# Kernel tuning notes

Measured on AMD Instinct MI355X. Metric: run time of the kernel, lower is better.

Reference implementation:

```python
import jax, jax.numpy as jnp
import numpy as np

N = 100000
E = 3200000
IN_C = 512
HID = 64
OP_C = 64
OUT_C = 2


def setup_inputs() -> dict:
    key = jax.random.key(0)
    ks = jax.random.split(key, 12)
    x = jax.random.normal(ks[0], (N, IN_C), dtype=jnp.float32)
    edge_index = jax.random.randint(ks[1], (2, E), 0, N, dtype=jnp.int32)
    edge_attr = jax.random.uniform(ks[2], (E,), dtype=jnp.float32)
    op = jax.random.normal(ks[3], (N, OP_C), dtype=jnp.float32)
    s1 = 1.0 / np.sqrt(IN_C)
    s2 = 1.0 / np.sqrt(HID)
    s3 = 1.0 / np.sqrt(IN_C + OP_C)
    W1 = jax.random.uniform(ks[4], (IN_C, HID), jnp.float32, -s1, s1)
    b1 = jnp.zeros((HID,), jnp.float32)
    W2 = jax.random.uniform(ks[5], (HID, HID), jnp.float32, -s2, s2)
    b2 = jnp.zeros((HID,), jnp.float32)
    Wp = jax.random.uniform(ks[6], (HID, IN_C), jnp.float32, -s2, s2)
    bp = jax.random.uniform(ks[7], (IN_C,), jnp.float32, -s2, s2)
    Wfc = jax.random.uniform(ks[8], (IN_C + OP_C, OUT_C), jnp.float32, -s3, s3)
    bfc = jax.random.uniform(ks[9], (OUT_C,), jnp.float32, -s3, s3)
    return {"x": x, "edge_index": edge_index, "edge_attr": edge_attr, "op": op,
            "W1": W1, "b1": b1, "W2": W2, "b2": b2,
            "Wp": Wp, "bp": bp, "Wfc": Wfc, "bfc": bfc}


def _gcn_conv(x, W, b, row, col, w):
    # PyG GCNConv: add self-loops (weight 1), symmetric normalization,
    # messages flow source(row) -> target(col).
    h = x @ W  # [N, out]
    loop = jnp.arange(N, dtype=row.dtype)
    row_f = jnp.concatenate([row, loop])
    col_f = jnp.concatenate([col, loop])
    w_f = jnp.concatenate([w, jnp.ones((N,), w.dtype)])
    deg = jax.ops.segment_sum(w_f, col_f, num_segments=N)
    dinv = jnp.where(deg > 0, jax.lax.rsqrt(jnp.maximum(deg, 1e-30)), 0.0)
    norm = dinv[row_f] * w_f * dinv[col_f]  # [E+N]
    msg = norm[:, None] * h[row_f]          # gather + weight
    out = jax.ops.segment_sum(msg, col_f, num_segments=N)  # scatter-add
    return out + b


def reference(x, edge_index, edge_attr, op, W1, b1, W2, b2, Wp, bp, Wfc, bfc):
    row, col = edge_index[0], edge_index[1]
    w = 1.0 / (edge_attr + 1.0)
    h = jax.nn.relu(_gcn_conv(x, W1, b1, row, col, w))   # dropout = identity (eval)
    h = jax.nn.relu(_gcn_conv(h, W2, b2, row, col, w))
    emb = h @ Wp + bp
    z = jnp.concatenate([emb, op], axis=1)
    return z @ Wfc + bfc
```

## Files before the change

kernel.cpp:

```cpp
#include <hip/hip_runtime.h>
#include <hip/hip_bf16.h>

#define IN_C 512
#define HID 64
#define OP_C 64
#define OUT_C 2

#define NPB 256
#define NPB_SHIFT 8
#define MAXB 512
#define BINB 1024
#define EPT 8
#define EPB (BINB*EPT)
#define WFIX 16777216.0f

using bf16x8 = __attribute__((ext_vector_type(8))) short;
using f32x4  = __attribute__((ext_vector_type(4))) float;

static __device__ __forceinline__ unsigned short f2bf(float f) {
    unsigned int u = __float_as_uint(f);
    u = (u + 0x7FFFu + ((u >> 16) & 1u)) >> 16;
    return (unsigned short)u;
}
static __device__ __forceinline__ short f2bf_hw(float f) {
    __bf16 h = (__bf16)f;
    return __builtin_bit_cast(short, h);
}
static __device__ __forceinline__ float bf2f(unsigned short s) {
    return __uint_as_float(((unsigned int)s) << 16);
}

static __device__ __forceinline__ unsigned long long pack_e(int src, int lc, float w) {
    return ((unsigned long long)lc << 49) | ((unsigned long long)(unsigned)src << 32)
         | (unsigned long long)__float_as_uint(w);
}

static __device__ __forceinline__ void wprep_one(const float* __restrict__ W,
                                                 unsigned short* __restrict__ wfrag, int idx) {
    int e  = idx & 7;
    int l  = (idx >> 3) & 63;
    int nf = (idx >> 9) & 3;
    int kt = idx >> 11;
    int k  = kt * 32 + (l >> 4) * 8 + e;
    int c  = nf * 16 + (l & 15);
    wfrag[idx] = f2bf(W[k * 64 + c]);
}

__global__ __launch_bounds__(256) void setup_k(const float* __restrict__ Wp,
                                               const float* __restrict__ bp,
                                               const float* __restrict__ Wfc,
                                               const float* __restrict__ bfc,
                                               float* M, float* cvec,
                                               const float* __restrict__ W1,
                                               unsigned short* __restrict__ wfrag1,
                                               const float* __restrict__ W2,
                                               unsigned short* __restrict__ wfrag2,
                                               int* gcnt, int B) {
    int b = blockIdx.x, t = threadIdx.x;
    if (b == 0) {
        if (t < 128) {
            int k = t >> 1, j = t & 1;
            float s = 0.f;
            for (int f = 0; f < IN_C; ++f) s += Wp[k * IN_C + f] * Wfc[f * 2 + j];
            M[t] = s;
        } else if (t < 130) {
            int j = t - 128;
            float s = bfc[j];
            for (int f = 0; f < IN_C; ++f) s += bp[f] * Wfc[f * 2 + j];
            cvec[j] = s;
        }
    } else if (b <= 128) {
        wprep_one(W1, wfrag1, (b - 1) * 256 + t);
    } else if (b <= 144) {
        wprep_one(W2, wfrag2, (b - 129) * 256 + t);
    } else {
        int i = (b - 145) * 256 + t;
        if (i < B) gcnt[i] = 0;
    }
}

__global__ __launch_bounds__(BINB) void p1a_k(const int* __restrict__ col,
                                              int* __restrict__ gcnt,
                                              int* __restrict__ blk_off,
                                              int E, int B) {
    __shared__ int hist[MAXB];
    int tid = threadIdx.x;
    long e0 = (long)blockIdx.x * EPB;
    for (int i = tid; i < B; i += BINB) hist[i] = 0;
    __syncthreads();
    #pragma unroll
    for (int j = 0; j < EPT; ++j) {
        long e = e0 + j * BINB + tid;
        if (e < E) atomicAdd(&hist[col[e] >> NPB_SHIFT], 1);
    }
    __syncthreads();
    for (int b = tid; b < B; b += BINB) {
        int h = hist[b];
        if (h > 0) blk_off[(long)blockIdx.x * B + b] = atomicAdd(&gcnt[b], h);
    }
}

__global__ __launch_bounds__(256) void scanB_k(const int* __restrict__ gcnt,
                                               int* __restrict__ bptr, int B, int E) {
    __shared__ int lds[256];
    int t = threadIdx.x;
    int v[4]; int s = 0;
    #pragma unroll
    for (int j = 0; j < 4; ++j) { int i = t * 4 + j; v[j] = (i < B) ? gcnt[i] : 0; s += v[j]; }
    lds[t] = s; __syncthreads();
    int x = s;
    for (int off = 1; off < 256; off <<= 1) {
        int y = (t >= off) ? lds[t - off] : 0;
        __syncthreads();
        x += y; lds[t] = x;
        __syncthreads();
    }
    int p = x - s;
    #pragma unroll
    for (int j = 0; j < 4; ++j) { int i = t * 4 + j; if (i < B) bptr[i] = p; p += v[j]; }
    if (t == 255) bptr[B] = E;
}

__global__ __launch_bounds__(BINB) void p1b_k(const int* __restrict__ row,
                                              const int* __restrict__ col,
                                              const float* __restrict__ attr,
                                              const int* __restrict__ blk_off,
                                              const int* __restrict__ bptr,
                                              unsigned long long* __restrict__ binned,
                                              int E, int B) {
    __shared__ int gbase[MAXB];
    __shared__ int loc[MAXB];
    __shared__ int scanb[512];
    __shared__ unsigned long long stage[EPB];
    int tid = threadIdx.x;
    int blk = blockIdx.x;
    long e0 = (long)blk * EPB;
    for (int i = tid; i < B; i += BINB) {
        gbase[i] = bptr[i] + blk_off[(long)blk * B + i];
        loc[i] = 0;
    }
    __syncthreads();
    unsigned long long pk[EPT]; int eb[EPT]; int er[EPT];
    #pragma unroll
    for (int j = 0; j < EPT; ++j) {
        long e = e0 + j * BINB + tid;
        eb[j] = -1;
        if (e < E) {
            int c = col[e];
            int b = c >> NPB_SHIFT;
            float w = 1.0f / (attr[e] + 1.0f);
            pk[j] = pack_e(row[e], c & (NPB - 1), w);
            eb[j] = b;
            er[j] = atomicAdd(&loc[b], 1);
        }
    }
    __syncthreads();
    if (tid < 512) scanb[tid] = (tid < B) ? loc[tid] : 0;
    __syncthreads();
    for (int off = 1; off < 512; off <<= 1) {
        int y = 0;
        if (tid < 512 && tid >= off) y = scanb[tid - off];
        __syncthreads();
        if (tid < 512) scanb[tid] += y;
        __syncthreads();
    }
    if (tid < B) loc[tid] = scanb[tid] - loc[tid];
    __syncthreads();
    #pragma unroll
    for (int j = 0; j < EPT; ++j)
        if (eb[j] >= 0) stage[loc[eb[j]] + er[j]] = pk[j];
    __syncthreads();
    long rem = E - e0;
    int ecnt = rem > EPB ? EPB : (int)rem;
    for (int i = tid; i < ecnt; i += BINB) {
        int lo = 0, hi = B - 1;
        #pragma unroll 1
        while (lo < hi) {
            int mid = (lo + hi + 1) >> 1;
            if (loc[mid] <= i) lo = mid; else hi = mid - 1;
        }
        binned[gbase[lo] + (i - loc[lo])] = stage[i];
    }
}

__global__ __launch_bounds__(256) void p2_k(const unsigned long long* __restrict__ binned,
                                            const int* __restrict__ bptr,
                                            int2* __restrict__ edges,
                                            int* __restrict__ rowptr,
                                            float* __restrict__ dinv,
                                            int N, int E) {
    __shared__ int cnt[NPB];
    __shared__ unsigned int fxw[NPB];
    __shared__ int excl[NPB];
    __shared__ int cur[NPB];
    __shared__ float dvl[NPB];
    int tid = threadIdx.x;
    int b = blockIdx.x;
    int e0 = bptr[b], e1 = bptr[b + 1];
    int c0 = b << NPB_SHIFT;
    cnt[tid] = 0; fxw[tid] = 0; cur[tid] = 0;
    if (b == 0 && tid == 0) rowptr[N] = E;
    __syncthreads();
    for (int i = e0 + tid; i < e1; i += 256) {
        unsigned long long p = binned[i];
        int lc = (int)(p >> 49);
        float w = __uint_as_float((unsigned int)p);
        atomicAdd(&cnt[lc], 1);
        atomicAdd(&fxw[lc], (unsigned int)(w * WFIX));
    }
    __syncthreads();
    excl[tid] = cnt[tid];
    __syncthreads();
    for (int off = 1; off < NPB; off <<= 1) {
        int v = (tid >= off) ? excl[tid - off] : 0;
        __syncthreads();
        excl[tid] += v;
        __syncthreads();
    }
    {
        int ex = excl[tid] - cnt[tid];
        excl[tid] = ex;
        int c = c0 + tid;
        if (c < N) {
            rowptr[c] = e0 + ex;
            float deg = 1.0f + (float)((double)fxw[tid] * (1.0 / 16777216.0));
            float dv = rsqrtf(deg);
            dinv[c] = dv;
            dvl[tid] = dv;
        }
    }
    __syncthreads();
    for (int i = e0 + tid; i < e1; i += 256) {
        unsigned long long p = binned[i];
        int lc = (int)(p >> 49);
        int src = (int)((p >> 32) & 0x1FFFF);
        float w = __uint_as_float((unsigned int)p);
        int r = atomicAdd(&cur[lc], 1);
        float nrm_p = w * dvl[lc];
        edges[e0 + excl[lc] + r] = make_int2(src, __float_as_int(nrm_p));
    }
}

__global__ __launch_bounds__(512) void gemm1_k(const float* __restrict__ A,
                                               const unsigned short* __restrict__ wfrag,
                                               const float* __restrict__ dinv,
                                               unsigned short* __restrict__ out, int M) {
    __shared__ unsigned short wlds[32768];
    int tid = threadIdx.x;
    {
        const float4* s4 = (const float4*)wfrag;
        float4* d4 = (float4*)wlds;
        #pragma unroll
        for (int i = 0; i < 8; ++i) d4[tid + 512 * i] = s4[tid + 512 * i];
    }
    __syncthreads();
    int wv = tid >> 6, l = tid & 63;
    int lg = l >> 4, lr = l & 15;
    long band = (long)blockIdx.x * 128 + wv * 16;
    long row = band + lr;
    long rowc = row < M ? row : (long)(M - 1);
    const float* xp = A + rowc * IN_C + lg * 8;
    f32x4 acc0 = {0.f,0.f,0.f,0.f}, acc1 = {0.f,0.f,0.f,0.f};
    f32x4 acc2 = {0.f,0.f,0.f,0.f}, acc3 = {0.f,0.f,0.f,0.f};
    #pragma unroll 4
    for (int kt = 0; kt < 16; ++kt) {
        float4 xa = *(const float4*)(xp + kt * 32);
        float4 xb = *(const float4*)(xp + kt * 32 + 4);
        bf16x8 a;
        a[0] = f2bf_hw(xa.x); a[1] = f2bf_hw(xa.y);
        a[2] = f2bf_hw(xa.z); a[3] = f2bf_hw(xa.w);
        a[4] = f2bf_hw(xb.x); a[5] = f2bf_hw(xb.y);
        a[6] = f2bf_hw(xb.z); a[7] = f2bf_hw(xb.w);
        const bf16x8* bp = (const bf16x8*)&wlds[kt * 4 * 64 * 8 + l * 8];
        acc0 = __builtin_amdgcn_mfma_f32_16x16x32_bf16(a, bp[0],   acc0, 0, 0, 0);
        acc1 = __builtin_amdgcn_mfma_f32_16x16x32_bf16(a, bp[64],  acc1, 0, 0, 0);
        acc2 = __builtin_amdgcn_mfma_f32_16x16x32_bf16(a, bp[128], acc2, 0, 0, 0);
        acc3 = __builtin_amdgcn_mfma_f32_16x16x32_bf16(a, bp[192], acc3, 0, 0, 0);
    }
    #pragma unroll
    for (int r = 0; r < 4; ++r) {
        long orow = band + lg * 4 + r;
        if (orow < M) {
            float dv = dinv[orow];
            out[orow * 64 +  0 + lr] = f2bf(acc0[r] * dv);
            out[orow * 64 + 16 + lr] = f2bf(acc1[r] * dv);
            out[orow * 64 + 32 + lr] = f2bf(acc2[r] * dv);
            out[orow * 64 + 48 + lr] = f2bf(acc3[r] * dv);
        }
    }
}

__global__ __launch_bounds__(512) void gemm2_k(const unsigned short* __restrict__ A2,
                                               const unsigned short* __restrict__ wfrag,
                                               const float* __restrict__ dinv,
                                               unsigned short* __restrict__ out, int M) {
    __shared__ unsigned short wlds[4096];
    int tid = threadIdx.x;
    ((float4*)wlds)[tid] = ((const float4*)wfrag)[tid];
    __syncthreads();
    int wv = tid >> 6, l = tid & 63;
    int lg = l >> 4, lr = l & 15;
    long band = (long)blockIdx.x * 128 + wv * 16;
    long row = band + lr;
    long rowc = row < M ? row : (long)(M - 1);
    const unsigned short* ap = A2 + rowc * 64 + lg * 8;
    f32x4 acc0 = {0.f,0.f,0.f,0.f}, acc1 = {0.f,0.f,0.f,0.f};
    f32x4 acc2 = {0.f,0.f,0.f,0.f}, acc3 = {0.f,0.f,0.f,0.f};
    #pragma unroll
    for (int kt = 0; kt < 2; ++kt) {
        bf16x8 a = *(const bf16x8*)(ap + kt * 32);
        const bf16x8* bp = (const bf16x8*)&wlds[kt * 4 * 64 * 8 + l * 8];
        acc0 = __builtin_amdgcn_mfma_f32_16x16x32_bf16(a, bp[0],   acc0, 0, 0, 0);
        acc1 = __builtin_amdgcn_mfma_f32_16x16x32_bf16(a, bp[64],  acc1, 0, 0, 0);
        acc2 = __builtin_amdgcn_mfma_f32_16x16x32_bf16(a, bp[128], acc2, 0, 0, 0);
        acc3 = __builtin_amdgcn_mfma_f32_16x16x32_bf16(a, bp[192], acc3, 0, 0, 0);
    }
    #pragma unroll
    for (int r = 0; r < 4; ++r) {
        long orow = band + lg * 4 + r;
        if (orow < M) {
            float dv = dinv[orow];
            out[orow * 64 +  0 + lr] = f2bf(acc0[r] * dv);
            out[orow * 64 + 16 + lr] = f2bf(acc1[r] * dv);
            out[orow * 64 + 32 + lr] = f2bf(acc2[r] * dv);
            out[orow * 64 + 48 + lr] = f2bf(acc3[r] * dv);
        }
    }
}

__device__ __forceinline__ void agg_core(const unsigned short* __restrict__ h2,
                                         const int* __restrict__ rowptr,
                                         const int2* __restrict__ edges,
                                         const float* __restrict__ dinv,
                                         const float* __restrict__ bias,
                                         int node, int l,
                                         float& acc0, float& acc1) {
    float di = dinv[node];
    ushort2 hv = *(const ushort2*)(h2 + (size_t)node * 64 + 2 * l);
    acc0 = di * bf2f(hv.x);
    acc1 = di * bf2f(hv.y);
    int s = rowptr[node], e = rowptr[node + 1];
    int li = l & 15;
    for (int base = s; base < e; base += 16) {
        int mm = e - base; mm = mm > 16 ? 16 : mm;
        int2 my = edges[base + (li < mm ? li : 0)];
        if (mm == 16) {
            #pragma unroll
            for (int j = 0; j < 16; ++j) {
                int srcj = __shfl(my.x, j, 32);
                float nj = __int_as_float(__shfl(my.y, j, 32));
                ushort2 q = *(const ushort2*)(h2 + (size_t)srcj * 64 + 2 * l);
                acc0 += nj * bf2f(q.x);
                acc1 += nj * bf2f(q.y);
            }
        } else {
            for (int j = 0; j < mm; ++j) {
                int srcj = __shfl(my.x, j, 32);
                float nj = __int_as_float(__shfl(my.y, j, 32));
                ushort2 q = *(const ushort2*)(h2 + (size_t)srcj * 64 + 2 * l);
                acc0 += nj * bf2f(q.x);
                acc1 += nj * bf2f(q.y);
            }
        }
    }
    float2 bb = *(const float2*)(bias + 2 * l);
    acc0 = fmaxf(acc0 + bb.x, 0.0f);
    acc1 = fmaxf(acc1 + bb.y, 0.0f);
}

__global__ __launch_bounds__(256) void agg1_k(const unsigned short* __restrict__ h2,
                                              unsigned short* __restrict__ g2,
                                              const int* __restrict__ rowptr,
                                              const int2* __restrict__ edges,
                                              const float* __restrict__ dinv,
                                              const float* __restrict__ bias, int N) {
    int wid = (blockIdx.x * 256 + threadIdx.x) >> 6;
    int lane = threadIdx.x & 63;
    int node = wid * 2 + (lane >> 5);
    int l = lane & 31;
    if (node >= N) return;
    float acc0, acc1;
    agg_core(h2, rowptr, edges, dinv, bias, node, l, acc0, acc1);
    ushort2 o; o.x = f2bf(acc0); o.y = f2bf(acc1);
    *(ushort2*)(g2 + (size_t)node * 64 + 2 * l) = o;
}

__global__ __launch_bounds__(256) void agg2f_k(const unsigned short* __restrict__ h2,
                                               const int* __restrict__ rowptr,
                                               const int2* __restrict__ edges,
                                               const float* __restrict__ dinv,
                                               const float* __restrict__ bias,
                                               const float* __restrict__ op,
                                               const float* __restrict__ M,
                                               const float* __restrict__ Wfc,
                                               const float* __restrict__ cvec,
                                               float* __restrict__ out, int N) {
    int wid = (blockIdx.x * 256 + threadIdx.x) >> 6;
    int lane = threadIdx.x & 63;
    int node = wid * 2 + (lane >> 5);
    int l = lane & 31;
    if (node >= N) return;
    float acc0, acc1;
    agg_core(h2, rowptr, edges, dinv, bias, node, l, acc0, acc1);
    float2 ov = *(const float2*)(op + (size_t)node * 64 + 2 * l);
    int f0 = 2 * l, f1 = 2 * l + 1;
    float p0 = acc0 * M[f0 * 2 + 0] + acc1 * M[f1 * 2 + 0]
             + ov.x * Wfc[(IN_C + f0) * 2 + 0] + ov.y * Wfc[(IN_C + f1) * 2 + 0];
    float p1 = acc0 * M[f0 * 2 + 1] + acc1 * M[f1 * 2 + 1]
             + ov.x * Wfc[(IN_C + f0) * 2 + 1] + ov.y * Wfc[(IN_C + f1) * 2 + 1];
    #pragma unroll
    for (int off = 16; off > 0; off >>= 1) {
        p0 += __shfl_xor(p0, off);
        p1 += __shfl_xor(p1, off);
    }
    if (l == 0)
        *(float2*)(out + (size_t)node * 2) = make_float2(p0 + cvec[0], p1 + cvec[1]);
}

extern "C" void kernel_launch(void* const* d_in, const int* in_sizes, int n_in,
                              void* d_out, int out_size, void* d_ws, size_t ws_size,
                              hipStream_t stream) {
    const float* x    = (const float*)d_in[0];
    const int*   ei   = (const int*)d_in[1];
    const float* attr = (const float*)d_in[2];
    const float* op   = (const float*)d_in[3];
    const float* W1   = (const float*)d_in[4];
    const float* b1   = (const float*)d_in[5];
    const float* W2   = (const float*)d_in[6];
    const float* b2   = (const float*)d_in[7];
    const float* Wp   = (const float*)d_in[8];
    const float* bp   = (const float*)d_in[9];
    const float* Wfc  = (const float*)d_in[10];
    const float* bfc  = (const float*)d_in[11];

    const int N = in_sizes[0] / IN_C;
    const int E = in_sizes[2];
    const int* row = ei;
    const int* col = ei + E;

    const int B     = (N + NPB - 1) >> NPB_SHIFT;
    const int nblk1 = (E + EPB - 1) / EPB;

    char* base = (char*)d_ws;
    size_t off = 0;
    auto alloc = [&](size_t bytes) -> char* {
        char* p = base + off;
        off = (off + bytes + 255) & ~(size_t)255;
        return p;
    };
    int2*  edges  = (int2*)alloc((size_t)E * 8);
    unsigned short* h2 = (unsigned short*)alloc((size_t)N * HID * 2);
    size_t bin_b  = (size_t)E * 8;
    size_t g_b    = (size_t)N * HID * 2;
    char*  regC   = alloc(bin_b > g_b ? bin_b : g_b);
    unsigned long long* binned = (unsigned long long*)regC;
    unsigned short* g2 = (unsigned short*)regC;
    int*   blkoff = (int*)alloc((size_t)nblk1 * B * 4);
    float* dinv   = (float*)alloc((size_t)N * 4);
    int*   rowptr = (int*)alloc((size_t)(N + 1) * 4);
    int*   gcnt   = (int*)alloc((size_t)MAXB * 4);
    int*   bptr   = (int*)alloc((size_t)(MAXB + 1) * 4);
    unsigned short* wfrag1 = (unsigned short*)alloc((size_t)IN_C * 64 * 2);
    unsigned short* wfrag2 = (unsigned short*)alloc((size_t)HID * 64 * 2);
    float* Mbuf   = (float*)alloc(512);
    float* cvec   = (float*)alloc(64);

    const int gAgg  = (((N + 1) / 2) * 64 + 255) / 256;
    const int gGemm = (N + 127) / 128;
    const int gSetup = 145 + (B + 255) / 256;

    setup_k<<<gSetup, 256, 0, stream>>>(Wp, bp, Wfc, bfc, Mbuf, cvec,
                                        W1, wfrag1, W2, wfrag2, gcnt, B);
    p1a_k<<<nblk1, BINB, 0, stream>>>(col, gcnt, blkoff, E, B);
    scanB_k<<<1, 256, 0, stream>>>(gcnt, bptr, B, E);
    p1b_k<<<nblk1, BINB, 0, stream>>>(row, col, attr, blkoff, bptr, binned, E, B);
    p2_k<<<B, 256, 0, stream>>>(binned, bptr, edges, rowptr, dinv, N, E);

    gemm1_k<<<gGemm, 512, 0, stream>>>(x, wfrag1, dinv, h2, N);
    agg1_k<<<gAgg, 256, 0, stream>>>(h2, g2, rowptr, edges, dinv, b1, N);
    gemm2_k<<<gGemm, 512, 0, stream>>>(g2, wfrag2, dinv, h2, N);
    agg2f_k<<<gAgg, 256, 0, stream>>>(h2, rowptr, edges, dinv, b2, op, Mbuf, Wfc, cvec,
                                      (float*)d_out, N);
}
```

Measured before the change: 305.3 us.

## Fuse layer-1 aggregation with layer-2 GEMM and fold bin scan into p1b

The standalone layer-1 aggregation kernel and the second GEMM are replaced by one kernel. It aggregates 16 nodes per block (16 lanes per node, 4 features per lane), stages the bf16 result in LDS and runs the 64x64 MFMA there, so the intermediate g2 no longer makes a round trip through global memory and one launch goes away. The single-block bin prefix scan is also removed: every p1b block now redoes the small scan over the bin counts, and block 0 writes bptr. The cost is redundant scan work in each p1b block and fewer lanes per node during aggregation, which changes the gather parallelism.

```diff
diff --git a/kernel.cpp b/kernel.cpp
--- a/kernel.cpp
+++ b/kernel.cpp
@@ -100,32 +100,12 @@
     }
 }
 
-__global__ __launch_bounds__(256) void scanB_k(const int* __restrict__ gcnt,
-                                               int* __restrict__ bptr, int B, int E) {
-    __shared__ int lds[256];
-    int t = threadIdx.x;
-    int v[4]; int s = 0;
-    #pragma unroll
-    for (int j = 0; j < 4; ++j) { int i = t * 4 + j; v[j] = (i < B) ? gcnt[i] : 0; s += v[j]; }
-    lds[t] = s; __syncthreads();
-    int x = s;
-    for (int off = 1; off < 256; off <<= 1) {
-        int y = (t >= off) ? lds[t - off] : 0;
-        __syncthreads();
-        x += y; lds[t] = x;
-        __syncthreads();
-    }
-    int p = x - s;
-    #pragma unroll
-    for (int j = 0; j < 4; ++j) { int i = t * 4 + j; if (i < B) bptr[i] = p; p += v[j]; }
-    if (t == 255) bptr[B] = E;
-}
-
 __global__ __launch_bounds__(BINB) void p1b_k(const int* __restrict__ row,
                                               const int* __restrict__ col,
                                               const float* __restrict__ attr,
                                               const int* __restrict__ blk_off,
-                                              const int* __restrict__ bptr,
+                                              const int* __restrict__ gcnt,
+                                              int* __restrict__ bptr_out,
                                               unsigned long long* __restrict__ binned,
                                               int E, int B) {
     __shared__ int gbase[MAXB];
@@ -135,10 +115,23 @@
     int tid = threadIdx.x;
     int blk = blockIdx.x;
     long e0 = (long)blk * EPB;
-    for (int i = tid; i < B; i += BINB) {
-        gbase[i] = bptr[i] + blk_off[(long)blk * B + i];
-        loc[i] = 0;
-    }
+    int gval = (tid < B) ? gcnt[tid] : 0;
+    if (tid < 512) scanb[tid] = gval;
+    __syncthreads();
+    for (int off = 1; off < 512; off <<= 1) {
+        int y = 0;
+        if (tid < 512 && tid >= off) y = scanb[tid - off];
+        __syncthreads();
+        if (tid < 512) scanb[tid] += y;
+        __syncthreads();
+    }
+    if (tid < B) {
+        int excl = scanb[tid] - gval;
+        gbase[tid] = excl + blk_off[(long)blk * B + tid];
+        loc[tid] = 0;
+        if (blk == 0) bptr_out[tid] = excl;
+    }
+    if (blk == 0 && tid == 0) bptr_out[B] = E;
     __syncthreads();
     unsigned long long pk[EPT]; int eb[EPT]; int er[EPT];
     #pragma unroll
@@ -290,40 +283,67 @@
     }
 }
 
-__global__ __launch_bounds__(512) void gemm2_k(const unsigned short* __restrict__ A2,
-                                               const unsigned short* __restrict__ wfrag,
+__global__ __launch_bounds__(256) void aggmm_k(const unsigned short* __restrict__ h2,
+                                               const unsigned short* __restrict__ wfrag2,
+                                               unsigned short* __restrict__ hout,
+                                               const int* __restrict__ rowptr,
+                                               const int2* __restrict__ edges,
                                                const float* __restrict__ dinv,
-                                               unsigned short* __restrict__ out, int M) {
-    __shared__ unsigned short wlds[4096];
+                                               const float* __restrict__ bias, int N) {
+    __shared__ unsigned short glds[16 * 64];
     int tid = threadIdx.x;
-    ((float4*)wlds)[tid] = ((const float4*)wfrag)[tid];
-    __syncthreads();
-    int wv = tid >> 6, l = tid & 63;
-    int lg = l >> 4, lr = l & 15;
-    long band = (long)blockIdx.x * 128 + wv * 16;
-    long row = band + lr;
-    long rowc = row < M ? row : (long)(M - 1);
-    const unsigned short* ap = A2 + rowc * 64 + lg * 8;
-    f32x4 acc0 = {0.f,0.f,0.f,0.f}, acc1 = {0.f,0.f,0.f,0.f};
-    f32x4 acc2 = {0.f,0.f,0.f,0.f}, acc3 = {0.f,0.f,0.f,0.f};
+    int w = tid >> 6, l = tid & 63;
+    int q = l >> 4, r = l & 15;
+    int node = blockIdx.x * 16 + w * 4 + q;
+    float a0 = 0.f, a1 = 0.f, a2 = 0.f, a3 = 0.f;
+    if (node < N) {
+        float di = dinv[node];
+        ushort4 hv = *(const ushort4*)(h2 + (size_t)node * 64 + 4 * r);
+        a0 = di * bf2f(hv.x); a1 = di * bf2f(hv.y);
+        a2 = di * bf2f(hv.z); a3 = di * bf2f(hv.w);
+        int s = rowptr[node], e = rowptr[node + 1];
+        for (int base = s; base < e; base += 16) {
+            int mm = e - base; mm = mm > 16 ? 16 : mm;
+            int2 my = edges[base + (r < mm ? r : 0)];
+            if (mm == 16) {
+                #pragma unroll
+                for (int j = 0; j < 16; ++j) {
+                    int srcj = __shfl(my.x, j, 16);
+                    float nj = __int_as_float(__shfl(my.y, j, 16));
+                    ushort4 qv = *(const ushort4*)(h2 + (size_t)srcj * 64 + 4 * r);
+                    a0 += nj * bf2f(qv.x); a1 += nj * bf2f(qv.y);
+                    a2 += nj * bf2f(qv.z); a3 += nj * bf2f(qv.w);
+                }
+            } else {
+                for (int j = 0; j < mm; ++j) {
+                    int srcj = __shfl(my.x, j, 16);
+                    float nj = __int_as_float(__shfl(my.y, j, 16));
+                    ushort4 qv = *(const ushort4*)(h2 + (size_t)srcj * 64 + 4 * r);
+                    a0 += nj * bf2f(qv.x); a1 += nj * bf2f(qv.y);
+                    a2 += nj * bf2f(qv.z); a3 += nj * bf2f(qv.w);
+                }
+            }
+        }
+        float4 bb = *(const float4*)(bias + 4 * r);
+        a0 = fmaxf(a0 + bb.x, 0.f); a1 = fmaxf(a1 + bb.y, 0.f);
+        a2 = fmaxf(a2 + bb.z, 0.f); a3 = fmaxf(a3 + bb.w, 0.f);
+    }
+    ushort4 gv; gv.x = f2bf(a0); gv.y = f2bf(a1); gv.z = f2bf(a2); gv.w = f2bf(a3);
+    *(ushort4*)&glds[(w * 4 + q) * 64 + 4 * r] = gv;
+    __syncthreads();
+    f32x4 acc = {0.f, 0.f, 0.f, 0.f};
     #pragma unroll
     for (int kt = 0; kt < 2; ++kt) {
-        bf16x8 a = *(const bf16x8*)(ap + kt * 32);
-        const bf16x8* bp = (const bf16x8*)&wlds[kt * 4 * 64 * 8 + l * 8];
-        acc0 = __builtin_amdgcn_mfma_f32_16x16x32_bf16(a, bp[0],   acc0, 0, 0, 0);
-        acc1 = __builtin_amdgcn_mfma_f32_16x16x32_bf16(a, bp[64],  acc1, 0, 0, 0);
-        acc2 = __builtin_amdgcn_mfma_f32_16x16x32_bf16(a, bp[128], acc2, 0, 0, 0);
-        acc3 = __builtin_amdgcn_mfma_f32_16x16x32_bf16(a, bp[192], acc3, 0, 0, 0);
-    }
-    #pragma unroll
-    for (int r = 0; r < 4; ++r) {
-        long orow = band + lg * 4 + r;
-        if (orow < M) {
-            float dv = dinv[orow];
-            out[orow * 64 +  0 + lr] = f2bf(acc0[r] * dv);
-            out[orow * 64 + 16 + lr] = f2bf(acc1[r] * dv);
-            out[orow * 64 + 32 + lr] = f2bf(acc2[r] * dv);
-            out[orow * 64 + 48 + lr] = f2bf(acc3[r] * dv);
+        bf16x8 afrag = *(const bf16x8*)&glds[(l & 15) * 64 + kt * 32 + (l >> 4) * 8];
+        bf16x8 bfrag = *(const bf16x8*)&wfrag2[(size_t)((kt * 4 + w) * 64 + l) * 8];
+        acc = __builtin_amdgcn_mfma_f32_16x16x32_bf16(afrag, bfrag, acc, 0, 0, 0);
+    }
+    #pragma unroll
+    for (int rr = 0; rr < 4; ++rr) {
+        int nrow = blockIdx.x * 16 + (l >> 4) * 4 + rr;
+        if (nrow < N) {
+            float dv = dinv[nrow];
+            hout[(size_t)nrow * 64 + w * 16 + (l & 15)] = f2bf(acc[rr] * dv);
         }
     }
 }
@@ -368,23 +388,6 @@
     acc1 = fmaxf(acc1 + bb.y, 0.0f);
 }
 
-__global__ __launch_bounds__(256) void agg1_k(const unsigned short* __restrict__ h2,
-                                              unsigned short* __restrict__ g2,
-                                              const int* __restrict__ rowptr,
-                                              const int2* __restrict__ edges,
-                                              const float* __restrict__ dinv,
-                                              const float* __restrict__ bias, int N) {
-    int wid = (blockIdx.x * 256 + threadIdx.x) >> 6;
-    int lane = threadIdx.x & 63;
-    int node = wid * 2 + (lane >> 5);
-    int l = lane & 31;
-    if (node >= N) return;
-    float acc0, acc1;
-    agg_core(h2, rowptr, edges, dinv, bias, node, l, acc0, acc1);
-    ushort2 o; o.x = f2bf(acc0); o.y = f2bf(acc1);
-    *(ushort2*)(g2 + (size_t)node * 64 + 2 * l) = o;
-}
-
 __global__ __launch_bounds__(256) void agg2f_k(const unsigned short* __restrict__ h2,
                                                const int* __restrict__ rowptr,
                                                const int2* __restrict__ edges,
@@ -454,7 +457,7 @@
     size_t g_b    = (size_t)N * HID * 2;
     char*  regC   = alloc(bin_b > g_b ? bin_b : g_b);
     unsigned long long* binned = (unsigned long long*)regC;
-    unsigned short* g2 = (unsigned short*)regC;
+    unsigned short* hout = (unsigned short*)regC;
     int*   blkoff = (int*)alloc((size_t)nblk1 * B * 4);
     float* dinv   = (float*)alloc((size_t)N * 4);
     int*   rowptr = (int*)alloc((size_t)(N + 1) * 4);
@@ -467,18 +470,17 @@
 
     const int gAgg  = (((N + 1) / 2) * 64 + 255) / 256;
     const int gGemm = (N + 127) / 128;
+    const int gAggmm = (N + 15) / 16;
     const int gSetup = 145 + (B + 255) / 256;
 
     setup_k<<<gSetup, 256, 0, stream>>>(Wp, bp, Wfc, bfc, Mbuf, cvec,
                                         W1, wfrag1, W2, wfrag2, gcnt, B);
     p1a_k<<<nblk1, BINB, 0, stream>>>(col, gcnt, blkoff, E, B);
-    scanB_k<<<1, 256, 0, stream>>>(gcnt, bptr, B, E);
-    p1b_k<<<nblk1, BINB, 0, stream>>>(row, col, attr, blkoff, bptr, binned, E, B);
+    p1b_k<<<nblk1, BINB, 0, stream>>>(row, col, attr, blkoff, gcnt, bptr, binned, E, B);
     p2_k<<<B, 256, 0, stream>>>(binned, bptr, edges, rowptr, dinv, N, E);
 
     gemm1_k<<<gGemm, 512, 0, stream>>>(x, wfrag1, dinv, h2, N);
-    agg1_k<<<gAgg, 256, 0, stream>>>(h2, g2, rowptr, edges, dinv, b1, N);
-    gemm2_k<<<gGemm, 512, 0, stream>>>(g2, wfrag2, dinv, h2, N);
-    agg2f_k<<<gAgg, 256, 0, stream>>>(h2, rowptr, edges, dinv, b2, op, Mbuf, Wfc, cvec,
+    aggmm_k<<<gAggmm, 256, 0, stream>>>(h2, wfrag2, hout, rowptr, edges, dinv, b1, N);
+    agg2f_k<<<gAgg, 256, 0, stream>>>(hout, rowptr, edges, dinv, b2, op, Mbuf, Wfc, cvec,
                                       (float*)d_out, N);
 }
```

Result: faster. 291.9 us (-4.4%).
